# Kernel tuning notes

Hardware: AMD Instinct MI355X
Metric: run time of the kernel (lower is better)

## Reference

```python
import jax, jax.numpy as jnp
import numpy as np

B_, J_, D_, E_, N_, K_ = 32, 1024, 192, 384, 16, 3


def _dwconv(x, w, b):
    # x: (B,J,E), w: (E,1,K) depthwise, b: (E,)
    xc = jnp.transpose(x, (0, 2, 1))  # (B,E,J)
    pad = w.shape[2] // 2
    y = jax.lax.conv_general_dilated(
        xc, w, window_strides=(1,), padding=[(pad, pad)],
        feature_group_count=w.shape[0], dimension_numbers=('NCH', 'OIH', 'NCH'))
    return jnp.transpose(y + b[None, :, None], (0, 2, 1))  # (B,J,E)


def _scan_dir(x, cw, cb, WB, bB, WC, bC, WD, bD, A, Wi, bi, Wr, br):
    # One directional selective-SSM pass. x: (B,J,E); A: (N,) negative diag.
    xc = _dwconv(x, cw, cb)                       # (B,J,E)
    Bt = xc @ WB + bB                             # (B,J,N)
    Ct = xc @ WC + bC                             # (B,J,N)
    Dt = jax.nn.softplus(xc @ WD + bD)            # Delta, (B,J,N)
    A_bar = jnp.exp(Dt * A)                       # ZOH discretization
    B_bar = (A_bar - 1.0) / (A + 1e-6) * Bt
    u = xc @ Wi + bi                              # in_to_state, (B,J,N)
    Bu = B_bar * u

    def step(h, ab_bu):
        ab, bu = ab_bu
        h = ab * h + bu
        return h, h

    h0 = jnp.zeros((x.shape[0], A.shape[0]), x.dtype)
    _, hs = jax.lax.scan(step, h0, (jnp.swapaxes(A_bar, 0, 1), jnp.swapaxes(Bu, 0, 1)))
    hs = jnp.swapaxes(hs, 0, 1)                   # (B,J,N)
    return (hs * Ct) @ Wr + br                    # readout, (B,J,E)


def setup_inputs() -> dict:
    key = jax.random.key(0)
    ks = iter(jax.random.split(key, 40))

    def nrm(shape, scale=0.02):
        return jax.random.normal(next(ks), shape, jnp.float32) * scale

    inp = {
        'tokens': jax.random.normal(next(ks), (B_, J_, D_), jnp.float32),
        'norm_g': jnp.ones((D_,), jnp.float32),
        'norm_b': jnp.zeros((D_,), jnp.float32),
        'Wx': nrm((D_, E_)), 'bx': jnp.zeros((E_,), jnp.float32),
        'Wz': nrm((D_, E_)), 'bz': jnp.zeros((E_,), jnp.float32),
        'convf_w': nrm((E_, 1, K_), 0.1), 'convf_b': jnp.zeros((E_,), jnp.float32),
        'convb_w': nrm((E_, 1, K_), 0.1), 'convb_b': jnp.zeros((E_,), jnp.float32),
        'WBf': nrm((E_, N_)), 'bBf': jnp.zeros((N_,), jnp.float32),
        'WCf': nrm((E_, N_)), 'bCf': jnp.zeros((N_,), jnp.float32),
        'WDf': nrm((E_, N_)), 'bDf': jnp.zeros((N_,), jnp.float32),
        'WBb': nrm((E_, N_)), 'bBb': jnp.zeros((N_,), jnp.float32),
        'WCb': nrm((E_, N_)), 'bCb': jnp.zeros((N_,), jnp.float32),
        'WDb': nrm((E_, N_)), 'bDb': jnp.zeros((N_,), jnp.float32),
        'A_log': nrm((N_,), 0.5),
        'Wi': nrm((E_, N_)), 'bi': jnp.zeros((N_,), jnp.float32),
        'Wr': nrm((N_, E_)), 'br': jnp.zeros((E_,), jnp.float32),
        'Wo': nrm((E_, D_)), 'bo': jnp.zeros((D_,), jnp.float32),
    }
    return inp


def reference(tokens, norm_g, norm_b, Wx, bx, Wz, bz, convf_w, convf_b,
              convb_w, convb_b, WBf, bBf, WCf, bCf, WDf, bDf, WBb, bBb,
              WCb, bCb, WDb, bDb, A_log, Wi, bi, Wr, br, Wo, bo):
    # LayerNorm (biased variance, eps=1e-5, like torch)
    mu = jnp.mean(tokens, axis=-1, keepdims=True)
    var = jnp.mean(jnp.square(tokens - mu), axis=-1, keepdims=True)
    t = (tokens - mu) / jnp.sqrt(var + 1e-5) * norm_g + norm_b

    x = t @ Wx + bx
    z = t @ Wz + bz
    gate = jax.nn.sigmoid(jax.nn.silu(z))

    # A computed under no_grad in torch -> stop_gradient here
    A = jax.lax.stop_gradient(-jax.nn.softplus(A_log))

    y_f = _scan_dir(x, convf_w, convf_b, WBf, bBf, WCf, bCf, WDf, bDf, A, Wi, bi, Wr, br)
    y_b = jnp.flip(_scan_dir(jnp.flip(x, 1), convb_w, convb_b, WBb, bBb, WCb, bCb,
                             WDb, bDb, A, Wi, bi, Wr, br), 1)
    y = (y_f + y_b) * gate
    return tokens + y @ Wo + bo
```

## Files before the change

### kernel.cpp

```cpp
#include <hip/hip_runtime.h>
#include <math.h>


typedef __attribute__((ext_vector_type(8))) short short8;
typedef __attribute__((ext_vector_type(4))) float f32x4;

__device__ __forceinline__ unsigned short f2bf(float f){
  union { float f; unsigned u; } v; v.f = f;
  unsigned r = v.u + 0x7FFFu + ((v.u >> 16) & 1u);
  return (unsigned short)(r >> 16);
}
__device__ __forceinline__ float bf2f(unsigned short s){
  union { unsigned u; float f; } v; v.u = ((unsigned)s) << 16;
  return v.f;
}
__device__ __forceinline__ float softplusf(float x){
  return (x > 20.f) ? x : log1pf(expf(x));
}
__device__ __forceinline__ float sigf_fast(float x){
  return __builtin_amdgcn_rcpf(1.f + __expf(-x));
}

__global__ __launch_bounds__(256) void prep_kernel(
    const float* __restrict__ Wx, const float* __restrict__ Wz,
    const float* __restrict__ WBf, const float* __restrict__ WCf,
    const float* __restrict__ WDf, const float* __restrict__ WBb,
    const float* __restrict__ WCb, const float* __restrict__ WDb,
    const float* __restrict__ Wi, const float* __restrict__ Wr,
    const float* __restrict__ Wo,
    const float* __restrict__ bBf, const float* __restrict__ bCf,
    const float* __restrict__ bDf, const float* __restrict__ bBb,
    const float* __restrict__ bCb, const float* __restrict__ bDb,
    const float* __restrict__ bi,
    unsigned short* __restrict__ Wxz_t, unsigned short* __restrict__ W4f_t,
    unsigned short* __restrict__ W4b_t, unsigned short* __restrict__ Wrt2,
    unsigned short* __restrict__ Wot, float* __restrict__ b4f,
    float* __restrict__ b4b)
{
  int idx = blockIdx.x * 256 + threadIdx.x;
  if (idx < 147456){ int n = idx / 192, k = idx % 192;
    Wxz_t[idx] = f2bf(n < 384 ? Wx[k*384 + n] : Wz[k*384 + n - 384]); return; }
  idx -= 147456;
  if (idx < 24576){ int n = idx / 384, k = idx % 384;
    const float* W = (n<16)?WBf:(n<32)?WCf:(n<48)?WDf:Wi;
    W4f_t[idx] = f2bf(W[k*16 + (n&15)]); return; }
  idx -= 24576;
  if (idx < 24576){ int n = idx / 384, k = idx % 384;
    const float* W = (n<16)?WBb:(n<32)?WCb:(n<48)?WDb:Wi;
    W4b_t[idx] = f2bf(W[k*16 + (n&15)]); return; }
  idx -= 24576;
  if (idx < 12288){ int n = idx / 32, k = idx % 32;
    Wrt2[idx] = f2bf(Wr[(k&15)*384 + n]); return; }
  idx -= 12288;
  if (idx < 73728){ int n = idx / 384, k = idx % 384;
    Wot[idx] = f2bf(Wo[k*192 + n]); return; }
  idx -= 73728;
  if (idx < 64){
    const float* bsel = (idx<16)?bBf:(idx<32)?bCf:(idx<48)?bDf:bi;
    b4f[idx] = bsel[idx & 15]; return; }
  idx -= 64;
  if (idx < 64){
    const float* bsel = (idx<16)?bBb:(idx<32)?bCb:(idx<48)?bDb:bi;
    b4b[idx] = bsel[idx & 15]; return; }
}

__global__ __launch_bounds__(256) void ln_kernel(
    const float* __restrict__ tokens, const float* __restrict__ g,
    const float* __restrict__ nb, unsigned short* __restrict__ t_bf)
{
  __shared__ unsigned short s[32 * 200];
  const int t = threadIdx.x;
  const int row0 = blockIdx.x * 32;
  {
    const int r = t >> 3, l8 = t & 7;
    const float* tr = tokens + (long)(row0 + r) * 192;
    float v[24], sm = 0.f, sq = 0.f;
#pragma unroll
    for (int i = 0; i < 24; i++){ float x = tr[l8 + 8*i]; v[i] = x; sm += x; sq += x*x; }
#pragma unroll
    for (int m = 1; m < 8; m <<= 1){ sm += __shfl_xor(sm, m); sq += __shfl_xor(sq, m); }
    const float mu = sm * (1.f/192.f);
    const float rstd = rsqrtf(sq * (1.f/192.f) - mu*mu + 1e-5f);
#pragma unroll
    for (int i = 0; i < 24; i++){
      const int d = l8 + 8*i;
      s[r*200 + d] = f2bf((v[i] - mu)*rstd*g[d] + nb[d]);
    }
  }
  __syncthreads();
  {
#pragma unroll
    for (int i = 0; i < 3; i++){
      const int item = i*256 + t;
      const int row = item / 24, c8 = item % 24;
      *(short8*)&t_bf[(long)(row0 + row)*192 + c8*8] =
          *(const short8*)&s[row*200 + c8*8];
    }
  }
}

__global__ __launch_bounds__(256) void xz_gemm(
    const unsigned short* __restrict__ t_bf,
    const unsigned short* __restrict__ Wxz_t,
    const float* __restrict__ bx, const float* __restrict__ bz,
    unsigned short* __restrict__ x_bf, unsigned short* __restrict__ gate_bf)
{
  __shared__ unsigned short tl[64 * 200];
  const int t = threadIdx.x;
  const int ct = blockIdx.x % 6;
  const int rt = blockIdx.x / 6;
  const int row0 = rt * 64;

  {
#pragma unroll
    for (int i = 0; i < 6; i++){
      const int item = i*256 + t;
      const int row = item / 24, c8 = item % 24;
      *(short8*)&tl[row*200 + c8*8] =
          *(const short8*)&t_bf[(long)(row0 + row)*192 + c8*8];
    }
  }
  __syncthreads();

  const int lane = t & 63, w = t >> 6;
  const int l15 = lane & 15, q = lane >> 4;
  const int C0 = ct*128 + w*32;

  f32x4 acc[4][2];
#pragma unroll
  for (int m = 0; m < 4; m++)
#pragma unroll
    for (int nf = 0; nf < 2; nf++) acc[m][nf] = (f32x4){0.f,0.f,0.f,0.f};

  const unsigned short* wb = Wxz_t + (long)(C0 + l15)*192 + q*8;
#pragma unroll
  for (int ks = 0; ks < 6; ks++){
    const int k0 = ks * 32;
    short8 a0 = *(const short8*)&tl[(     l15)*200 + k0 + q*8];
    short8 a1 = *(const short8*)&tl[(16 + l15)*200 + k0 + q*8];
    short8 a2 = *(const short8*)&tl[(32 + l15)*200 + k0 + q*8];
    short8 a3 = *(const short8*)&tl[(48 + l15)*200 + k0 + q*8];
#pragma unroll
    for (int nf = 0; nf < 2; nf++){
      short8 bw = *(const short8*)&wb[nf*16*192 + k0];
      acc[0][nf] = __builtin_amdgcn_mfma_f32_16x16x32_bf16(a0, bw, acc[0][nf], 0, 0, 0);
      acc[1][nf] = __builtin_amdgcn_mfma_f32_16x16x32_bf16(a1, bw, acc[1][nf], 0, 0, 0);
      acc[2][nf] = __builtin_amdgcn_mfma_f32_16x16x32_bf16(a2, bw, acc[2][nf], 0, 0, 0);
      acc[3][nf] = __builtin_amdgcn_mfma_f32_16x16x32_bf16(a3, bw, acc[3][nf], 0, 0, 0);
    }
  }
  __syncthreads();

  unsigned short* stg = tl;
  const int isgate = (ct >= 3);
#pragma unroll
  for (int nf = 0; nf < 2; nf++){
    const int c = C0 + nf*16 + l15;
    const float bv = isgate ? bz[c - 384] : bx[c];
#pragma unroll
    for (int m = 0; m < 4; m++){
#pragma unroll
      for (int r = 0; r < 4; r++){
        float val = acc[m][nf][r] + bv;
        if (isgate){ const float si = val * sigf_fast(val); val = sigf_fast(si); }
        stg[(m*16 + q*4 + r)*136 + (w*32 + nf*16 + l15)] = f2bf(val);
      }
    }
  }
  __syncthreads();

  {
    unsigned short* outp = isgate ? gate_bf : x_bf;
    const int cb = isgate ? (ct*128 - 384) : (ct*128);
#pragma unroll
    for (int i = 0; i < 4; i++){
      const int item = i*256 + t;
      const int row = item / 16, c8 = item % 16;
      *(short8*)&outp[(long)(row0 + row)*384 + cb + c8*8] =
          *(const short8*)&stg[row*136 + c8*8];
    }
  }
}

__global__ __launch_bounds__(256) void proj_mfma(
    const unsigned short* __restrict__ x_bf,
    const float* __restrict__ cwf, const float* __restrict__ cbf,
    const float* __restrict__ cwb, const float* __restrict__ cbb,
    const unsigned short* __restrict__ W4f, const unsigned short* __restrict__ W4b,
    const float* __restrict__ b4f, const float* __restrict__ b4b,
    const float* __restrict__ A_log,
    float* __restrict__ Af, float* __restrict__ Buf, float* __restrict__ Ctf,
    float* __restrict__ Ab, float* __restrict__ Bub, float* __restrict__ Ctb)
{
  __shared__ unsigned short xc[64 * 392];
  float* trans = (float*)xc;
  const int t = threadIdx.x;
  const int dir = blockIdx.x >> 9;
  const int bid = blockIdx.x & 511;
  const int b  = bid >> 4;
  const int j0 = (bid & 15) * 64;
  const float* cw = dir ? cwb : cwf;
  const float* cb = dir ? cbb : cbf;
  const unsigned short* W4 = dir ? W4b : W4f;
  const float* b4 = dir ? b4b : b4f;
  float* Aout = dir ? Ab  : Af;
  float* Bout = dir ? Bub : Buf;
  float* Cout = dir ? Ctb : Ctf;

  {
    const long xrow = (long)b * 1024 * 384;
#pragma unroll
    for (int i = 0; i < 12; i++){
      const int idx = i*256 + t;
      const int r = idx / 48;
      const int e0 = (idx - r*48) * 8;
      const int jp = j0 + r;
      short8 xm = (short8){0,0,0,0,0,0,0,0};
      short8 xp = (short8){0,0,0,0,0,0,0,0};
      if (jp >= 1){
        const int js = dir ? 1024 - jp : jp - 1;
        xm = *(const short8*)&x_bf[xrow + (long)js*384 + e0];
      }
      short8 x0;
      {
        const int js = dir ? 1023 - jp : jp;
        x0 = *(const short8*)&x_bf[xrow + (long)js*384 + e0];
      }
      if (jp <= 1022){
        const int js = dir ? 1022 - jp : jp + 1;
        xp = *(const short8*)&x_bf[xrow + (long)js*384 + e0];
      }
      float wv[24], cbv[8];
#pragma unroll
      for (int v = 0; v < 6; v++)
        *(float4*)&wv[v*4] = *(const float4*)&cw[e0*3 + v*4];
#pragma unroll
      for (int v = 0; v < 2; v++)
        *(float4*)&cbv[v*4] = *(const float4*)&cb[e0 + v*4];
      short8 o;
#pragma unroll
      for (int m = 0; m < 8; m++){
        const float acc = fmaf(wv[3*m],   bf2f((unsigned short)xm[m]),
                          fmaf(wv[3*m+1], bf2f((unsigned short)x0[m]),
                          fmaf(wv[3*m+2], bf2f((unsigned short)xp[m]), cbv[m])));
        o[m] = (short)f2bf(acc);
      }
      *(short8*)&xc[r*392 + e0] = o;
    }
  }
  __syncthreads();

  const int lane = t & 63, w = t >> 6;
  const int l15 = lane & 15, q = lane >> 4;
  f32x4 acc[4];
#pragma unroll
  for (int nf = 0; nf < 4; nf++) acc[nf] = (f32x4){0.f,0.f,0.f,0.f};
  const unsigned short* wb = W4 + (long)l15*384 + q*8;
#pragma unroll
  for (int ks = 0; ks < 12; ks++){
    const int k0 = ks * 32;
    short8 a = *(const short8*)&xc[(w*16 + l15)*392 + k0 + q*8];
#pragma unroll
    for (int nf = 0; nf < 4; nf++){
      short8 bw = *(const short8*)&wb[nf*16*384 + k0];
      acc[nf] = __builtin_amdgcn_mfma_f32_16x16x32_bf16(a, bw, acc[nf], 0, 0, 0);
    }
  }
  __syncthreads();

  {
    const int n = l15;
    const float Av = -softplusf(A_log[n]);
    const float bB = b4[n], bC = b4[16+n], bD = b4[32+n], bU = b4[48+n];
#pragma unroll
    for (int r = 0; r < 4; r++){
      const int row = w*16 + q*4 + r;
      const float Bt  = acc[0][r] + bB;
      const float Ctv = acc[1][r] + bC;
      const float dt  = softplusf(acc[2][r] + bD);
      const float u   = acc[3][r] + bU;
      const float ab  = expf(dt * Av);
      const float bu  = (ab - 1.f) / (Av + 1e-6f) * Bt * u;
      trans[(0*16 + n)*66 + row] = ab;
      trans[(1*16 + n)*66 + row] = bu;
      trans[(2*16 + n)*66 + row] = Ctv;
    }
  }
  __syncthreads();

  {
    const int j = t & 63, n4 = t >> 6;
#pragma unroll
    for (int i = 0; i < 4; i++){
      const int n = n4*4 + i;
      const int jp = j0 + j;
      const long base = ((long)b*16 + n) * 1024;
      Aout[base + jp] = trans[(0*16 + n)*66 + j];
      Bout[base + jp] = trans[(1*16 + n)*66 + j];
      Cout[base + (dir ? 1023 - jp : jp)] = trans[(2*16 + n)*66 + j];
    }
  }
}

__global__ __launch_bounds__(256) void scan2_kernel(
    const float* __restrict__ Af, const float* __restrict__ Buf, float* __restrict__ hsf,
    const float* __restrict__ Ab, const float* __restrict__ Bub, float* __restrict__ hsb)
{
  __shared__ float sA[256], sB[256];
  const int sel = blockIdx.x >> 9;
  const long base = (long)(blockIdx.x & 511) * 1024;
  const float* Abar = sel ? Ab  : Af;
  const float* Bu   = sel ? Bub : Buf;
  float* hs         = sel ? hsb : hsf;
  const int t = threadIdx.x;
  const float4 a4 = *reinterpret_cast<const float4*>(&Abar[base + t*4]);
  const float4 b4 = *reinterpret_cast<const float4*>(&Bu[base + t*4]);
  float A = a4.x, Bc = b4.x;
  Bc = fmaf(a4.y, Bc, b4.y); A *= a4.y;
  Bc = fmaf(a4.z, Bc, b4.z); A *= a4.z;
  Bc = fmaf(a4.w, Bc, b4.w); A *= a4.w;
  sA[t] = A; sB[t] = Bc;
  __syncthreads();
  for (int off = 1; off < 256; off <<= 1){
    const float cA = sA[t], cB = sB[t];
    float pA = 1.f, pB = 0.f;
    if (t >= off){ pA = sA[t - off]; pB = sB[t - off]; }
    __syncthreads();
    sA[t] = pA * cA;
    sB[t] = fmaf(cA, pB, cB);
    __syncthreads();
  }
  float h = (t > 0) ? sB[t - 1] : 0.f;
  float4 o;
  h = fmaf(a4.x, h, b4.x); o.x = h;
  h = fmaf(a4.y, h, b4.y); o.y = h;
  h = fmaf(a4.z, h, b4.z); o.z = h;
  h = fmaf(a4.w, h, b4.w); o.w = h;
  *reinterpret_cast<float4*>(&hs[base + t*4]) = o;
}

__global__ __launch_bounds__(256) void final_mfma(
    const float* __restrict__ tokens, const unsigned short* __restrict__ gate_bf,
    const float* __restrict__ hsf, const float* __restrict__ Ctf,
    const float* __restrict__ hsb, const float* __restrict__ Ctb,
    const unsigned short* __restrict__ Wrt2, const float* __restrict__ br,
    const unsigned short* __restrict__ Wot, const float* __restrict__ bo,
    float* __restrict__ out)
{
  __shared__ unsigned short s2[32 * 40];
  __shared__ unsigned short yg[32 * 392];
  const int t = threadIdx.x;
  const int b  = blockIdx.x >> 5;
  const int j0 = (blockIdx.x & 31) * 32;

  {
#pragma unroll
    for (int i = 0; i < 4; i++){
      const int idx = i*256 + t;
      const int j = idx & 31, kk = idx >> 5;
      float val;
      if (kk < 16){
        const long p = ((long)b*16 + kk)*1024 + j0 + j;
        val = hsf[p] * Ctf[p];
      } else {
        const long basen = ((long)b*16 + (kk - 16)) * 1024;
        val = hsb[basen + 1023 - (j0 + j)] * Ctb[basen + j0 + j];
      }
      s2[j*40 + kk] = f2bf(val);
    }
  }
  __syncthreads();

  const int lane = t & 63, w = t >> 6;
  const int l15 = lane & 15, q = lane >> 4;
  const int rt = w & 1;
  const int ng = w >> 1;

  {
    short8 a = *(const short8*)&s2[(rt*16 + l15)*40 + q*8];
    const unsigned short* wbp = Wrt2 + (long)l15*32 + q*8;
#pragma unroll
    for (int i = 0; i < 12; i++){
      const int nf = ng*12 + i;
      short8 bw = *(const short8*)&wbp[nf*16*32];
      f32x4 acc = (f32x4){0.f,0.f,0.f,0.f};
      acc = __builtin_amdgcn_mfma_f32_16x16x32_bf16(a, bw, acc, 0, 0, 0);
      const int c = nf*16 + l15;
      const float brv = 2.f * br[c];
#pragma unroll
      for (int r = 0; r < 4; r++)
        yg[(rt*16 + q*4 + r)*392 + c] = f2bf(acc[r] + brv);
    }
  }
  __syncthreads();

  {
#pragma unroll
    for (int i = 0; i < 6; i++){
      const int item = i*256 + t;
      const int row = item / 48;
      const int cb  = (item % 48) * 8;
      short8 y8 = *(const short8*)&yg[row*392 + cb];
      short8 g8 = *(const short8*)&gate_bf[((long)b*1024 + j0 + row)*384 + cb];
      short8 o;
#pragma unroll
      for (int m = 0; m < 8; m++)
        o[m] = (short)f2bf(bf2f((unsigned short)y8[m]) * bf2f((unsigned short)g8[m]));
      *(short8*)&yg[row*392 + cb] = o;
    }
  }
  __syncthreads();

  f32x4 acc[6];
  {
#pragma unroll
    for (int i = 0; i < 6; i++) acc[i] = (f32x4){0.f,0.f,0.f,0.f};
    const unsigned short* wbp = Wot + (long)l15*384 + q*8;
#pragma unroll
    for (int ks = 0; ks < 12; ks++){
      const int k0 = ks * 32;
      short8 a = *(const short8*)&yg[(rt*16 + l15)*392 + k0 + q*8];
#pragma unroll
      for (int i = 0; i < 6; i++){
        const int nf = ng*6 + i;
        short8 bw = *(const short8*)&wbp[(long)nf*16*384 + k0];
        acc[i] = __builtin_amdgcn_mfma_f32_16x16x32_bf16(a, bw, acc[i], 0, 0, 0);
      }
    }
  }
  __syncthreads();

  float* stg = (float*)yg;
  {
    const int gq = q ^ (q >> 1);
#pragma unroll
    for (int i = 0; i < 6; i++){
      const int nf = ng*6 + i;
      const int c = nf*16 + l15;
      const float bv = bo[c];
      const int scol = ((nf + gq) % 12)*16 + l15;
#pragma unroll
      for (int r = 0; r < 4; r++)
        stg[(rt*16 + q*4 + r)*196 + scol] = acc[i][r] + bv;
    }
  }
  __syncthreads();

  {
#pragma unroll
    for (int i = 0; i < 6; i++){
      const int item = i*256 + t;
      const int row = item / 48;
      const int c4  = (item % 48) * 4;
      const int qq = (row >> 2) & 3;
      const int gg = qq ^ (qq >> 1);
      const int nf = c4 / 16;
      const int scol = ((nf + gg) % 12)*16 + (c4 % 16);
      float4 v = *(const float4*)&stg[row*196 + scol];
      const long R = (long)b*1024 + j0 + row;
      const float4 tk = *(const float4*)&tokens[R*192 + c4];
      v.x += tk.x; v.y += tk.y; v.z += tk.z; v.w += tk.w;
      *(float4*)&out[R*192 + c4] = v;
    }
  }
}

extern "C" void kernel_launch(void* const* d_in, const int* in_sizes, int n_in,
                              void* d_out, int out_size, void* d_ws, size_t ws_size,
                              hipStream_t stream)
{
  const float* tokens  = (const float*)d_in[0];
  const float* norm_g  = (const float*)d_in[1];
  const float* norm_b  = (const float*)d_in[2];
  const float* Wx      = (const float*)d_in[3];
  const float* bx      = (const float*)d_in[4];
  const float* Wz      = (const float*)d_in[5];
  const float* bz      = (const float*)d_in[6];
  const float* convf_w = (const float*)d_in[7];
  const float* convf_b = (const float*)d_in[8];
  const float* convb_w = (const float*)d_in[9];
  const float* convb_b = (const float*)d_in[10];
  const float* WBf     = (const float*)d_in[11];
  const float* bBf     = (const float*)d_in[12];
  const float* WCf     = (const float*)d_in[13];
  const float* bCf     = (const float*)d_in[14];
  const float* WDf     = (const float*)d_in[15];
  const float* bDf     = (const float*)d_in[16];
  const float* WBb     = (const float*)d_in[17];
  const float* bBb     = (const float*)d_in[18];
  const float* WCb     = (const float*)d_in[19];
  const float* bCb     = (const float*)d_in[20];
  const float* WDb     = (const float*)d_in[21];
  const float* bDb     = (const float*)d_in[22];
  const float* A_log   = (const float*)d_in[23];
  const float* Wi      = (const float*)d_in[24];
  const float* bi      = (const float*)d_in[25];
  const float* Wr      = (const float*)d_in[26];
  const float* br      = (const float*)d_in[27];
  const float* Wo      = (const float*)d_in[28];
  const float* bo      = (const float*)d_in[29];

  char* ws = (char*)d_ws;
  unsigned short* x_bf    = (unsigned short*)(ws + 0);
  unsigned short* gate_bf = (unsigned short*)(ws + 25165824);
  unsigned short* Wxz_t   = (unsigned short*)(ws + 50331648);
  unsigned short* W4f_t   = (unsigned short*)(ws + 50626560);
  unsigned short* W4b_t   = (unsigned short*)(ws + 50675712);
  unsigned short* Wrt2    = (unsigned short*)(ws + 50724864);
  unsigned short* Wot     = (unsigned short*)(ws + 50749440);
  float* b4f = (float*)(ws + 50896896);
  float* b4b = (float*)(ws + 50897152);
  float* Af  = (float*)(ws + 50897408);
  float* Buf = (float*)(ws + 52994560);
  float* Ctf = (float*)(ws + 55091712);
  float* hsf = (float*)(ws + 57188864);
  float* Ab  = (float*)(ws + 59286016);
  float* Bub = (float*)(ws + 61383168);
  float* Ctb = (float*)(ws + 63480320);
  float* hsb = (float*)(ws + 65577472);
  unsigned short* t_bf = (unsigned short*)(ws + 67674624);

  prep_kernel<<<1105, 256, 0, stream>>>(Wx, Wz, WBf, WCf, WDf, WBb, WCb, WDb,
                                        Wi, Wr, Wo, bBf, bCf, bDf, bBb, bCb, bDb, bi,
                                        Wxz_t, W4f_t, W4b_t, Wrt2, Wot, b4f, b4b);
  ln_kernel<<<1024, 256, 0, stream>>>(tokens, norm_g, norm_b, t_bf);
  xz_gemm<<<3072, 256, 0, stream>>>(t_bf, Wxz_t, bx, bz, x_bf, gate_bf);
  proj_mfma<<<1024, 256, 0, stream>>>(x_bf, convf_w, convf_b, convb_w, convb_b,
                                      W4f_t, W4b_t, b4f, b4b, A_log,
                                      Af, Buf, Ctf, Ab, Bub, Ctb);
  scan2_kernel<<<1024, 256, 0, stream>>>(Af, Buf, hsf, Ab, Bub, hsb);
  final_mfma<<<1024, 256, 0, stream>>>(tokens, gate_bf, hsf, Ctf, hsb, Ctb,
                                       Wrt2, br, Wot, bo, (float*)d_out);
}
```

Baseline: 141.5 us.

## Halve final kernel row tile, batch conv loads, use fast math in projection

The final readout/output-projection kernel now handles 16 rows per block instead of 32, launches twice as many blocks, and uses smaller shared-memory tiles with new padding. Each wave covers a slice of output columns rather than a row-half. The intent is to raise occupancy and parallelism, at the cost of reloading the weight tiles for each block. In proj_mfma, the depthwise-conv input loads are grouped into two batches of six to improve memory-level parallelism, and softplus/exp/divide are replaced with fast intrinsics and a reciprocal, at a small accuracy cost.

```diff
diff --git a/kernel.cpp b/kernel.cpp
--- a/kernel.cpp
+++ b/kernel.cpp
@@ -16,6 +16,9 @@
 }
 __device__ __forceinline__ float softplusf(float x){
   return (x > 20.f) ? x : log1pf(expf(x));
+}
+__device__ __forceinline__ float softplus_fast(float x){
+  return (x > 20.f) ? x : __logf(1.f + __expf(x));
 }
 __device__ __forceinline__ float sigf_fast(float x){
   return __builtin_amdgcn_rcpf(1.f + __expf(-x));
@@ -210,42 +213,51 @@
   {
     const long xrow = (long)b * 1024 * 384;
 #pragma unroll
-    for (int i = 0; i < 12; i++){
-      const int idx = i*256 + t;
-      const int r = idx / 48;
-      const int e0 = (idx - r*48) * 8;
-      const int jp = j0 + r;
-      short8 xm = (short8){0,0,0,0,0,0,0,0};
-      short8 xp = (short8){0,0,0,0,0,0,0,0};
-      if (jp >= 1){
-        const int js = dir ? 1024 - jp : jp - 1;
-        xm = *(const short8*)&x_bf[xrow + (long)js*384 + e0];
+    for (int half = 0; half < 2; half++){
+      short8 xmv[6], x0v[6], xpv[6];
+#pragma unroll
+      for (int i = 0; i < 6; i++){
+        const int idx = (half*6 + i)*256 + t;
+        const int r = idx / 48;
+        const int e0 = (idx - r*48) * 8;
+        const int jp = j0 + r;
+        xmv[i] = (short8){0,0,0,0,0,0,0,0};
+        xpv[i] = (short8){0,0,0,0,0,0,0,0};
+        if (jp >= 1){
+          const int js = dir ? 1024 - jp : jp - 1;
+          xmv[i] = *(const short8*)&x_bf[xrow + (long)js*384 + e0];
+        }
+        {
+          const int js = dir ? 1023 - jp : jp;
+          x0v[i] = *(const short8*)&x_bf[xrow + (long)js*384 + e0];
+        }
+        if (jp <= 1022){
+          const int js = dir ? 1022 - jp : jp + 1;
+          xpv[i] = *(const short8*)&x_bf[xrow + (long)js*384 + e0];
+        }
       }
-      short8 x0;
-      {
-        const int js = dir ? 1023 - jp : jp;
-        x0 = *(const short8*)&x_bf[xrow + (long)js*384 + e0];
+#pragma unroll
+      for (int i = 0; i < 6; i++){
+        const int idx = (half*6 + i)*256 + t;
+        const int r = idx / 48;
+        const int e0 = (idx - r*48) * 8;
+        float wv[24], cbv[8];
+#pragma unroll
+        for (int v = 0; v < 6; v++)
+          *(float4*)&wv[v*4] = *(const float4*)&cw[e0*3 + v*4];
+#pragma unroll
+        for (int v = 0; v < 2; v++)
+          *(float4*)&cbv[v*4] = *(const float4*)&cb[e0 + v*4];
+        short8 o;
+#pragma unroll
+        for (int m = 0; m < 8; m++){
+          const float acc = fmaf(wv[3*m],   bf2f((unsigned short)xmv[i][m]),
+                            fmaf(wv[3*m+1], bf2f((unsigned short)x0v[i][m]),
+                            fmaf(wv[3*m+2], bf2f((unsigned short)xpv[i][m]), cbv[m])));
+          o[m] = (short)f2bf(acc);
+        }
+        *(short8*)&xc[r*392 + e0] = o;
       }
-      if (jp <= 1022){
-        const int js = dir ? 1022 - jp : jp + 1;
-        xp = *(const short8*)&x_bf[xrow + (long)js*384 + e0];
-      }
-      float wv[24], cbv[8];
-#pragma unroll
-      for (int v = 0; v < 6; v++)
-        *(float4*)&wv[v*4] = *(const float4*)&cw[e0*3 + v*4];
-#pragma unroll
-      for (int v = 0; v < 2; v++)
-        *(float4*)&cbv[v*4] = *(const float4*)&cb[e0 + v*4];
-      short8 o;
-#pragma unroll
-      for (int m = 0; m < 8; m++){
-        const float acc = fmaf(wv[3*m],   bf2f((unsigned short)xm[m]),
-                          fmaf(wv[3*m+1], bf2f((unsigned short)x0[m]),
-                          fmaf(wv[3*m+2], bf2f((unsigned short)xp[m]), cbv[m])));
-        o[m] = (short)f2bf(acc);
-      }
-      *(short8*)&xc[r*392 + e0] = o;
     }
   }
   __syncthreads();
@@ -272,15 +284,16 @@
     const int n = l15;
     const float Av = -softplusf(A_log[n]);
     const float bB = b4[n], bC = b4[16+n], bD = b4[32+n], bU = b4[48+n];
+    const float rAv = __builtin_amdgcn_rcpf(Av + 1e-6f);
 #pragma unroll
     for (int r = 0; r < 4; r++){
       const int row = w*16 + q*4 + r;
       const float Bt  = acc[0][r] + bB;
       const float Ctv = acc[1][r] + bC;
-      const float dt  = softplusf(acc[2][r] + bD);
+      const float dt  = softplus_fast(acc[2][r] + bD);
       const float u   = acc[3][r] + bU;
-      const float ab  = expf(dt * Av);
-      const float bu  = (ab - 1.f) / (Av + 1e-6f) * Bt * u;
+      const float ab  = __expf(dt * Av);
+      const float bu  = (ab - 1.f) * rAv * Bt * u;
       trans[(0*16 + n)*66 + row] = ab;
       trans[(1*16 + n)*66 + row] = bu;
       trans[(2*16 + n)*66 + row] = Ctv;
@@ -347,17 +360,18 @@
     const unsigned short* __restrict__ Wot, const float* __restrict__ bo,
     float* __restrict__ out)
 {
-  __shared__ unsigned short s2[32 * 40];
-  __shared__ unsigned short yg[32 * 392];
+  __shared__ unsigned short s2[16 * 36];
+  __shared__ float stgf[16 * 200];
+  unsigned short* yg = (unsigned short*)stgf;
   const int t = threadIdx.x;
-  const int b  = blockIdx.x >> 5;
-  const int j0 = (blockIdx.x & 31) * 32;
-
-  {
-#pragma unroll
-    for (int i = 0; i < 4; i++){
+  const int b  = blockIdx.x >> 6;
+  const int j0 = (blockIdx.x & 63) * 16;
+
+  {
+#pragma unroll
+    for (int i = 0; i < 2; i++){
       const int idx = i*256 + t;
-      const int j = idx & 31, kk = idx >> 5;
+      const int j = idx & 15, kk = idx >> 4;
       float val;
       if (kk < 16){
         const long p = ((long)b*16 + kk)*1024 + j0 + j;
@@ -366,22 +380,20 @@
         const long basen = ((long)b*16 + (kk - 16)) * 1024;
         val = hsb[basen + 1023 - (j0 + j)] * Ctb[basen + j0 + j];
       }
-      s2[j*40 + kk] = f2bf(val);
+      s2[j*36 + kk] = f2bf(val);
     }
   }
   __syncthreads();
 
   const int lane = t & 63, w = t >> 6;
   const int l15 = lane & 15, q = lane >> 4;
-  const int rt = w & 1;
-  const int ng = w >> 1;
-
-  {
-    short8 a = *(const short8*)&s2[(rt*16 + l15)*40 + q*8];
+
+  {
+    short8 a = *(const short8*)&s2[l15*36 + q*8];
     const unsigned short* wbp = Wrt2 + (long)l15*32 + q*8;
 #pragma unroll
-    for (int i = 0; i < 12; i++){
-      const int nf = ng*12 + i;
+    for (int i = 0; i < 6; i++){
+      const int nf = w*6 + i;
       short8 bw = *(const short8*)&wbp[nf*16*32];
       f32x4 acc = (f32x4){0.f,0.f,0.f,0.f};
       acc = __builtin_amdgcn_mfma_f32_16x16x32_bf16(a, bw, acc, 0, 0, 0);
@@ -389,40 +401,40 @@
       const float brv = 2.f * br[c];
 #pragma unroll
       for (int r = 0; r < 4; r++)
-        yg[(rt*16 + q*4 + r)*392 + c] = f2bf(acc[r] + brv);
-    }
-  }
-  __syncthreads();
-
-  {
-#pragma unroll
-    for (int i = 0; i < 6; i++){
+        yg[(q*4 + r)*388 + c] = f2bf(acc[r] + brv);
+    }
+  }
+  __syncthreads();
+
+  {
+#pragma unroll
+    for (int i = 0; i < 3; i++){
       const int item = i*256 + t;
       const int row = item / 48;
       const int cb  = (item % 48) * 8;
-      short8 y8 = *(const short8*)&yg[row*392 + cb];
+      short8 y8 = *(const short8*)&yg[row*388 + cb];
       short8 g8 = *(const short8*)&gate_bf[((long)b*1024 + j0 + row)*384 + cb];
       short8 o;
 #pragma unroll
       for (int m = 0; m < 8; m++)
         o[m] = (short)f2bf(bf2f((unsigned short)y8[m]) * bf2f((unsigned short)g8[m]));
-      *(short8*)&yg[row*392 + cb] = o;
-    }
-  }
-  __syncthreads();
-
-  f32x4 acc[6];
-  {
-#pragma unroll
-    for (int i = 0; i < 6; i++) acc[i] = (f32x4){0.f,0.f,0.f,0.f};
+      *(short8*)&yg[row*388 + cb] = o;
+    }
+  }
+  __syncthreads();
+
+  f32x4 acc[3];
+  {
+#pragma unroll
+    for (int i = 0; i < 3; i++) acc[i] = (f32x4){0.f,0.f,0.f,0.f};
     const unsigned short* wbp = Wot + (long)l15*384 + q*8;
 #pragma unroll
     for (int ks = 0; ks < 12; ks++){
       const int k0 = ks * 32;
-      short8 a = *(const short8*)&yg[(rt*16 + l15)*392 + k0 + q*8];
-#pragma unroll
-      for (int i = 0; i < 6; i++){
-        const int nf = ng*6 + i;
+      short8 a = *(const short8*)&yg[l15*388 + k0 + q*8];
+#pragma unroll
+      for (int i = 0; i < 3; i++){
+        const int nf = w*3 + i;
         short8 bw = *(const short8*)&wbp[(long)nf*16*384 + k0];
         acc[i] = __builtin_amdgcn_mfma_f32_16x16x32_bf16(a, bw, acc[i], 0, 0, 0);
       }
@@ -430,25 +442,24 @@
   }
   __syncthreads();
 
-  float* stg = (float*)yg;
   {
     const int gq = q ^ (q >> 1);
 #pragma unroll
-    for (int i = 0; i < 6; i++){
-      const int nf = ng*6 + i;
+    for (int i = 0; i < 3; i++){
+      const int nf = w*3 + i;
       const int c = nf*16 + l15;
       const float bv = bo[c];
       const int scol = ((nf + gq) % 12)*16 + l15;
 #pragma unroll
       for (int r = 0; r < 4; r++)
-        stg[(rt*16 + q*4 + r)*196 + scol] = acc[i][r] + bv;
-    }
-  }
-  __syncthreads();
-
-  {
-#pragma unroll
-    for (int i = 0; i < 6; i++){
+        stgf[(q*4 + r)*200 + scol] = acc[i][r] + bv;
+    }
+  }
+  __syncthreads();
+
+  {
+#pragma unroll
+    for (int i = 0; i < 3; i++){
       const int item = i*256 + t;
       const int row = item / 48;
       const int c4  = (item % 48) * 4;
@@ -456,7 +467,7 @@
       const int gg = qq ^ (qq >> 1);
       const int nf = c4 / 16;
       const int scol = ((nf + gg) % 12)*16 + (c4 % 16);
-      float4 v = *(const float4*)&stg[row*196 + scol];
+      float4 v = *(const float4*)&stgf[row*200 + scol];
       const long R = (long)b*1024 + j0 + row;
       const float4 tk = *(const float4*)&tokens[R*192 + c4];
       v.x += tk.x; v.y += tk.y; v.z += tk.z; v.w += tk.w;
@@ -529,6 +540,6 @@
                                       W4f_t, W4b_t, b4f, b4b, A_log,
                                       Af, Buf, Ctf, Ab, Bub, Ctb);
   scan2_kernel<<<1024, 256, 0, stream>>>(Af, Buf, hsf, Ab, Bub, hsb);
-  final_mfma<<<1024, 256, 0, stream>>>(tokens, gate_bf, hsf, Ctf, hsb, Ctb,
+  final_mfma<<<2048, 256, 0, stream>>>(tokens, gate_bf, hsf, Ctf, hsb, Ctb,
                                        Wrt2, br, Wot, bo, (float*)d_out);
 }
```

Measured after the change: 143.8 us. No clear change (+1.6%).
